# Kernel tuning notes

Measured on AMD Instinct MI355X. Metric: run time of the kernel, lower is better.

## Reference

```python
import jax, jax.numpy as jnp
import numpy as np

FEAT_DIM = 128
TIME_DIM = 128
D_MODEL = FEAT_DIM + TIME_DIM  # 256
N_HEAD = 2
D_K = D_MODEL // N_HEAD  # 128
B, N = 4096, 64


def setup_inputs() -> dict:
    key = jax.random.key(0)
    ks = jax.random.split(key, 16)
    s = lambda k, sh, sc=0.05: jax.random.normal(k, sh, dtype=jnp.float32) * sc
    return {
        "src": jax.random.normal(ks[0], (B, FEAT_DIM), dtype=jnp.float32),
        "src_t": jax.random.normal(ks[1], (B, 1, TIME_DIM), dtype=jnp.float32),
        "seq": jax.random.normal(ks[2], (B, N, FEAT_DIM), dtype=jnp.float32),
        "seq_t": jax.random.normal(ks[3], (B, N, TIME_DIM), dtype=jnp.float32),
        "mask": jax.random.randint(ks[4], (B, N), 0, 2).astype(jnp.bool_),
        # attention params (x @ W convention, W: [d_model, n_head*d_k])
        "w_qs": s(ks[5], (D_MODEL, N_HEAD * D_K)),
        "w_ks": s(ks[6], (D_MODEL, N_HEAD * D_K)),
        "w_vs": s(ks[7], (D_MODEL, N_HEAD * D_K)),
        "fc_w": s(ks[8], (N_HEAD * D_K, D_MODEL)),
        "fc_b": jnp.zeros((D_MODEL,), jnp.float32),
        "ln_g": jnp.ones((D_MODEL,), jnp.float32),
        "ln_b": jnp.zeros((D_MODEL,), jnp.float32),
        # MergeLayer params: fc1 [(d_model+feat), feat], fc2 [feat, feat]
        "fc1_w": s(ks[9], (D_MODEL + FEAT_DIM, FEAT_DIM)),
        "fc1_b": jnp.zeros((FEAT_DIM,), jnp.float32),
        "fc2_w": s(ks[10], (FEAT_DIM, FEAT_DIM)),
        "fc2_b": jnp.zeros((FEAT_DIM,), jnp.float32),
    }


def _layer_norm(x, g, b, eps=1e-5):
    mu = jnp.mean(x, axis=-1, keepdims=True)
    var = jnp.mean((x - mu) ** 2, axis=-1, keepdims=True)
    return (x - mu) * jax.lax.rsqrt(var + eps) * g + b


def reference(src, src_t, seq, seq_t, mask,
              w_qs, w_ks, w_vs, fc_w, fc_b, ln_g, ln_b,
              fc1_w, fc1_b, fc2_w, fc2_b):
    # q: [B,1,D_MODEL] = cat(src, src_t); k=v: [B,N,D_MODEL]
    q_in = jnp.concatenate([src[:, None, :], src_t], axis=2)
    k_in = jnp.concatenate([seq, seq_t], axis=2)

    q = (q_in @ w_qs).reshape(B, 1, N_HEAD, D_K)   # [B,1,H,dk]
    k = (k_in @ w_ks).reshape(B, N, N_HEAD, D_K)   # [B,N,H,dk]
    v = (k_in @ w_vs).reshape(B, N, N_HEAD, D_K)   # [B,N,H,dv]

    # scaled dot-product attention, len_q == 1
    attn = jnp.einsum('bqhd,bkhd->bhqk', q, k) / jnp.sqrt(jnp.float32(D_K))
    attn = jnp.where(mask[:, None, None, :], jnp.float32(-1e10), attn)
    attn = jax.nn.softmax(attn, axis=-1)           # [B,H,1,N]

    out = jnp.einsum('bhqk,bkhd->bqhd', attn, v).reshape(B, 1, N_HEAD * D_K)
    out = out @ fc_w + fc_b                         # dropout is identity (eval)
    out = _layer_norm(out + q_in, ln_g, ln_b)       # [B,1,D_MODEL]

    out = out[:, 0, :]                              # squeeze -> [B,D_MODEL]
    # MergeLayer: cat(out, src) -> fc1 -> relu -> fc2
    h = jnp.concatenate([out, src], axis=1)
    h = jax.nn.relu(h @ fc1_w + fc1_b)
    merged = h @ fc2_w + fc2_b                      # [B, FEAT_DIM]

    # attn squeeze: [n_head*B, N] ordering matches torch view(n_head, B, ...)
    attn_sq = jnp.transpose(attn[:, :, 0, :], (1, 0, 2)).reshape(N_HEAD * B, N)
    return merged, attn_sq
```

## Files before the change

### kernel.cpp

```cpp
#include <hip/hip_runtime.h>


__device__ __forceinline__ void fma4(float4& a, float s, const float4& w) {
  a.x = fmaf(s, w.x, a.x); a.y = fmaf(s, w.y, a.y);
  a.z = fmaf(s, w.z, a.z); a.w = fmaf(s, w.w, a.w);
}
__device__ __forceinline__ float dot4(const float4& a, const float4& b) {
  return a.x * b.x + a.y * b.y + a.z * b.z + a.w * b.w;
}

__global__ __launch_bounds__(256) void k_qproj(const float* __restrict__ src,
                                               const float* __restrict__ srct,
                                               const float* __restrict__ w_qs,
                                               float* __restrict__ Q) {
  __shared__ float sQ[16 * 256];
  const int tid = threadIdx.x;
  const int rb = blockIdx.x * 16;
  {
    const int r = tid >> 4;
    const int cb = (tid & 15) * 16;
#pragma unroll
    for (int i = 0; i < 4; ++i) {
      const int c = cb + i * 4;
      float4 v = (c < 128) ? *(const float4*)&src[(rb + r) * 128 + c]
                           : *(const float4*)&srct[(rb + r) * 128 + (c - 128)];
      *(float4*)&sQ[r * 256 + c] = v;
    }
  }
  __syncthreads();
  const int rg = tid >> 6;
  const int cg = tid & 63;
  float4 acc[4] = {};
  for (int k = 0; k < 256; k += 4) {
    const float4 w0 = *(const float4*)&w_qs[(k + 0) * 256 + cg * 4];
    const float4 w1 = *(const float4*)&w_qs[(k + 1) * 256 + cg * 4];
    const float4 w2 = *(const float4*)&w_qs[(k + 2) * 256 + cg * 4];
    const float4 w3 = *(const float4*)&w_qs[(k + 3) * 256 + cg * 4];
#pragma unroll
    for (int r = 0; r < 4; ++r) {
      const float4 a = *(const float4*)&sQ[(rg * 4 + r) * 256 + k];
      fma4(acc[r], a.x, w0); fma4(acc[r], a.y, w1);
      fma4(acc[r], a.z, w2); fma4(acc[r], a.w, w3);
    }
  }
#pragma unroll
  for (int r = 0; r < 4; ++r)
    *(float4*)&Q[(rb + rg * 4 + r) * 256 + cg * 4] = acc[r];
}

__global__ __launch_bounds__(256) void k_qkproj(const float* __restrict__ Q,
                                                const float* __restrict__ w_ks,
                                                float* __restrict__ QK) {
  __shared__ float sQ[8 * 256];
  const int tid = threadIdx.x;
  const int rb = blockIdx.x * 8;
#pragma unroll
  for (int i = 0; i < 2; ++i) {
    const int f4 = i * 256 + tid;
    const int r = f4 >> 6;
    const int c = (f4 & 63) * 4;
    *(float4*)&sQ[r * 256 + c] = *(const float4*)&Q[(rb + r) * 256 + c];
  }
  __syncthreads();
  const int rg = tid >> 7;
  const int cg = tid & 127;
  const int h = cg >> 6;
  const int j0 = (cg * 4) & 255;
  float4 acc[4] = {};
  for (int t = 0; t < 128; t += 4) {
    const float4 w0 = *(const float4*)&w_ks[(j0 + 0) * 256 + h * 128 + t];
    const float4 w1 = *(const float4*)&w_ks[(j0 + 1) * 256 + h * 128 + t];
    const float4 w2 = *(const float4*)&w_ks[(j0 + 2) * 256 + h * 128 + t];
    const float4 w3 = *(const float4*)&w_ks[(j0 + 3) * 256 + h * 128 + t];
#pragma unroll
    for (int r = 0; r < 4; ++r) {
      const float4 a = *(const float4*)&sQ[(rg * 4 + r) * 256 + h * 128 + t];
      acc[r].x += dot4(a, w0);
      acc[r].y += dot4(a, w1);
      acc[r].z += dot4(a, w2);
      acc[r].w += dot4(a, w3);
    }
  }
#pragma unroll
  for (int r = 0; r < 4; ++r)
    *(float4*)&QK[(rb + rg * 4 + r) * 512 + cg * 4] = acc[r];
}

__global__ __launch_bounds__(256) void k_attn(const float* __restrict__ seq,
                                              const float* __restrict__ seqt,
                                              const unsigned int* __restrict__ mw,
                                              float* QKS,
                                              float* __restrict__ att) {
  const int tid = threadIdx.x;
  const int lane = tid & 63;
  const int b = blockIdx.x * 4 + (tid >> 6);
  const int mv = (mw[b * 64 + lane] != 0u) ? 1 : 0;
  const float* kin = (lane < 32) ? (seq + b * 8192 + lane * 4)
                                 : (seqt + b * 8192 + (lane - 32) * 4);
  const float4 qk0 = *(const float4*)(QKS + b * 512 + lane * 4);
  const float4 qk1 = *(const float4*)(QKS + b * 512 + 256 + lane * 4);
  float4 s0 = {0.f, 0.f, 0.f, 0.f}, s1 = {0.f, 0.f, 0.f, 0.f};
  float l0 = 0.f, l1 = 0.f, rex0 = 0.f, rex1 = 0.f;
  const float scale = 0.08838834764831845f;
#pragma unroll 8
  for (int n = 0; n < 64; ++n) {
    const float4 kv = *(const float4*)(kin + n * 128);
    float p0 = dot4(kv, qk0);
    float p1 = dot4(kv, qk1);
#pragma unroll
    for (int off = 32; off >= 1; off >>= 1) {
      p0 += __shfl_xor(p0, off);
      p1 += __shfl_xor(p1, off);
    }
    const int mn = __shfl(mv, n);
    const float e0 = mn ? 0.f : __expf(p0 * scale);
    const float e1 = mn ? 0.f : __expf(p1 * scale);
    l0 += e0; l1 += e1;
    fma4(s0, e0, kv);
    fma4(s1, e1, kv);
    rex0 = (lane == n) ? e0 : rex0;
    rex1 = (lane == n) ? e1 : rex1;
  }
  const float i0 = 1.0f / l0;
  const float i1 = 1.0f / l1;
  const float4 o0 = {s0.x * i0, s0.y * i0, s0.z * i0, s0.w * i0};
  const float4 o1 = {s1.x * i1, s1.y * i1, s1.z * i1, s1.w * i1};
  *(float4*)(QKS + b * 512 + lane * 4) = o0;
  *(float4*)(QKS + b * 512 + 256 + lane * 4) = o1;
  att[b * 64 + lane] = rex0 * i0;
  att[4096 * 64 + b * 64 + lane] = rex1 * i1;
}

__global__ __launch_bounds__(256) void k_epi(
    const float* __restrict__ S, const float* __restrict__ src,
    const float* __restrict__ srct, const float* __restrict__ w_vs,
    const float* __restrict__ fc_w, const float* __restrict__ fc_b,
    const float* __restrict__ ln_g, const float* __restrict__ ln_b,
    const float* __restrict__ fc1_w, const float* __restrict__ fc1_b,
    const float* __restrict__ fc2_w, const float* __restrict__ fc2_b,
    float* __restrict__ out) {
  __shared__ float sv[4][512];
  __shared__ float qin[4][256];
  __shared__ float ov[4][256];
  __shared__ float xx[4][256];
  __shared__ float hcat[4][384];
  __shared__ float h1[4][128];
  __shared__ float stats[4][2];
  const int tid = threadIdx.x;
  const int b0 = blockIdx.x * 4;

#pragma unroll
  for (int i = 0; i < 2; ++i) {
    const int f4 = i * 256 + tid;
    const int g = f4 >> 7;
    const int c = (f4 & 127) * 4;
    *(float4*)&sv[g][c] = *(const float4*)&S[(b0 + g) * 512 + c];
  }
  {
    const int g = tid >> 6;
    const int c = (tid & 63) * 4;
    float4 v = (c < 128) ? *(const float4*)&src[(b0 + g) * 128 + c]
                         : *(const float4*)&srct[(b0 + g) * 128 + (c - 128)];
    *(float4*)&qin[g][c] = v;
  }
  __syncthreads();

  {
    const int h = tid >> 7;
    float acc[4] = {0.f, 0.f, 0.f, 0.f};
    for (int t = 0; t < 256; ++t) {
      const float w = w_vs[t * 256 + tid];
#pragma unroll
      for (int g = 0; g < 4; ++g) acc[g] = fmaf(sv[g][h * 256 + t], w, acc[g]);
    }
#pragma unroll
    for (int g = 0; g < 4; ++g) ov[g][tid] = acc[g];
  }
  __syncthreads();

  {
    float acc[4] = {0.f, 0.f, 0.f, 0.f};
    for (int d = 0; d < 256; ++d) {
      const float w = fc_w[d * 256 + tid];
#pragma unroll
      for (int g = 0; g < 4; ++g) acc[g] = fmaf(ov[g][d], w, acc[g]);
    }
    const float fb = fc_b[tid];
#pragma unroll
    for (int g = 0; g < 4; ++g) xx[g][tid] = acc[g] + fb + qin[g][tid];
  }
  __syncthreads();

  if (tid < 4) {
    const int g = tid;
    float s = 0.f, ss = 0.f;
    for (int j = 0; j < 256; ++j) {
      const float x = xx[g][j];
      s += x; ss += x * x;
    }
    const float mu = s * (1.0f / 256.0f);
    const float var = ss * (1.0f / 256.0f) - mu * mu;
    stats[g][0] = mu;
    stats[g][1] = rsqrtf(var + 1e-5f);
  }
  __syncthreads();
  {
    const float gg = ln_g[tid], bb = ln_b[tid];
#pragma unroll
    for (int g = 0; g < 4; ++g)
      hcat[g][tid] = (xx[g][tid] - stats[g][0]) * stats[g][1] * gg + bb;
  }
#pragma unroll
  for (int i = 0; i < 2; ++i) {
    const int idx = i * 256 + tid;
    const int g = idx >> 7, c = idx & 127;
    hcat[g][256 + c] = src[(b0 + g) * 128 + c];
  }
  __syncthreads();

  {
    const int col = tid & 127;
    const int gp = (tid >> 7) * 2;
    float acc0 = fc1_b[col], acc1 = acc0;
    for (int d = 0; d < 384; ++d) {
      const float w = fc1_w[d * 128 + col];
      acc0 = fmaf(hcat[gp][d], w, acc0);
      acc1 = fmaf(hcat[gp + 1][d], w, acc1);
    }
    h1[gp][col] = fmaxf(acc0, 0.f);
    h1[gp + 1][col] = fmaxf(acc1, 0.f);
  }
  __syncthreads();

  {
    const int col = tid & 127;
    const int gp = (tid >> 7) * 2;
    float acc0 = fc2_b[col], acc1 = acc0;
    for (int d = 0; d < 128; ++d) {
      const float w = fc2_w[d * 128 + col];
      acc0 = fmaf(h1[gp][d], w, acc0);
      acc1 = fmaf(h1[gp + 1][d], w, acc1);
    }
    out[(b0 + gp) * 128 + col] = acc0;
    out[(b0 + gp + 1) * 128 + col] = acc1;
  }
}

extern "C" void kernel_launch(void* const* d_in, const int* in_sizes, int n_in,
                              void* d_out, int out_size, void* d_ws,
                              size_t ws_size, hipStream_t stream) {
  (void)in_sizes; (void)n_in; (void)out_size; (void)ws_size;
  const float* src = (const float*)d_in[0];
  const float* srct = (const float*)d_in[1];
  const float* seq = (const float*)d_in[2];
  const float* seqt = (const float*)d_in[3];
  const unsigned int* mask = (const unsigned int*)d_in[4];
  const float* w_qs = (const float*)d_in[5];
  const float* w_ks = (const float*)d_in[6];
  const float* w_vs = (const float*)d_in[7];
  const float* fc_w = (const float*)d_in[8];
  const float* fc_b = (const float*)d_in[9];
  const float* ln_g = (const float*)d_in[10];
  const float* ln_b = (const float*)d_in[11];
  const float* fc1_w = (const float*)d_in[12];
  const float* fc1_b = (const float*)d_in[13];
  const float* fc2_w = (const float*)d_in[14];
  const float* fc2_b = (const float*)d_in[15];
  float* out = (float*)d_out;
  float* att = out + 4096 * 128;
  float* Q = (float*)d_ws;
  float* QKS = Q + 4096 * 256;
  k_qproj<<<256, 256, 0, stream>>>(src, srct, w_qs, Q);
  k_qkproj<<<512, 256, 0, stream>>>(Q, w_ks, QKS);
  k_attn<<<1024, 256, 0, stream>>>(seq, seqt, mask, QKS, att);
  k_epi<<<1024, 256, 0, stream>>>(QKS, src, srct, w_vs, fc_w, fc_b, ln_g,
                                  ln_b, fc1_w, fc1_b, fc2_w, fc2_b, out);
}
```

Baseline: 466.6 us.

## Fold Wq·Wkᵀ into one weight and restructure attention to skip masked keys

Precomputes a fused 256x512 weight W = Wq_h·Wk_hᵀ·scale per call, so the query-key projection becomes a single GEMM from the concatenated inputs instead of two chained projections. The attention kernel now computes each key's score with one lane per key (no per-key wave reductions), normalizes once, and accumulates the weighted sum only over unmasked keys using a ballot-compacted index list. This removes the 64 serial shuffle reductions per row and roughly halves the value-accumulation loads for the random mask, at the cost of an extra small weight-fusion kernel and strided per-lane row reads in the score pass. The softmax omits max-subtraction, which the old code also did.

```diff
diff --git a/kernel.cpp b/kernel.cpp
--- a/kernel.cpp
+++ b/kernel.cpp
@@ -9,13 +9,31 @@
   return a.x * b.x + a.y * b.y + a.z * b.z + a.w * b.w;
 }
 
-__global__ __launch_bounds__(256) void k_qproj(const float* __restrict__ src,
-                                               const float* __restrict__ srct,
-                                               const float* __restrict__ w_qs,
-                                               float* __restrict__ Q) {
+__global__ __launch_bounds__(256) void k_wf(const float* __restrict__ w_qs,
+                                            const float* __restrict__ w_ks,
+                                            float* __restrict__ W) {
+  const int idx = blockIdx.x * 256 + threadIdx.x;
+  const int c = idx >> 9;
+  const int col = idx & 511;
+  const int h = col >> 8;
+  const int j = col & 255;
+  const float* a = w_qs + c * 256 + h * 128;
+  const float* bk = w_ks + j * 256 + h * 128;
+  float acc = 0.f;
+#pragma unroll
+  for (int d = 0; d < 128; d += 4)
+    acc += dot4(*(const float4*)&a[d], *(const float4*)&bk[d]);
+  W[idx] = acc * 0.08838834764831845f;
+}
+
+__global__ __launch_bounds__(256) void k_qk(const float* __restrict__ src,
+                                            const float* __restrict__ srct,
+                                            const float* __restrict__ W,
+                                            float* __restrict__ QK) {
   __shared__ float sQ[16 * 256];
   const int tid = threadIdx.x;
-  const int rb = blockIdx.x * 16;
+  const int rb = (blockIdx.x >> 1) * 16;
+  const int ch = (blockIdx.x & 1) * 256;
   {
     const int r = tid >> 4;
     const int cb = (tid & 15) * 16;
@@ -30,12 +48,13 @@
   __syncthreads();
   const int rg = tid >> 6;
   const int cg = tid & 63;
+  const int col = ch + cg * 4;
   float4 acc[4] = {};
   for (int k = 0; k < 256; k += 4) {
-    const float4 w0 = *(const float4*)&w_qs[(k + 0) * 256 + cg * 4];
-    const float4 w1 = *(const float4*)&w_qs[(k + 1) * 256 + cg * 4];
-    const float4 w2 = *(const float4*)&w_qs[(k + 2) * 256 + cg * 4];
-    const float4 w3 = *(const float4*)&w_qs[(k + 3) * 256 + cg * 4];
+    const float4 w0 = *(const float4*)&W[(k + 0) * 512 + col];
+    const float4 w1 = *(const float4*)&W[(k + 1) * 512 + col];
+    const float4 w2 = *(const float4*)&W[(k + 2) * 512 + col];
+    const float4 w3 = *(const float4*)&W[(k + 3) * 512 + col];
 #pragma unroll
     for (int r = 0; r < 4; ++r) {
       const float4 a = *(const float4*)&sQ[(rg * 4 + r) * 256 + k];
@@ -45,45 +64,7 @@
   }
 #pragma unroll
   for (int r = 0; r < 4; ++r)
-    *(float4*)&Q[(rb + rg * 4 + r) * 256 + cg * 4] = acc[r];
-}
-
-__global__ __launch_bounds__(256) void k_qkproj(const float* __restrict__ Q,
-                                                const float* __restrict__ w_ks,
-                                                float* __restrict__ QK) {
-  __shared__ float sQ[8 * 256];
-  const int tid = threadIdx.x;
-  const int rb = blockIdx.x * 8;
-#pragma unroll
-  for (int i = 0; i < 2; ++i) {
-    const int f4 = i * 256 + tid;
-    const int r = f4 >> 6;
-    const int c = (f4 & 63) * 4;
-    *(float4*)&sQ[r * 256 + c] = *(const float4*)&Q[(rb + r) * 256 + c];
-  }
-  __syncthreads();
-  const int rg = tid >> 7;
-  const int cg = tid & 127;
-  const int h = cg >> 6;
-  const int j0 = (cg * 4) & 255;
-  float4 acc[4] = {};
-  for (int t = 0; t < 128; t += 4) {
-    const float4 w0 = *(const float4*)&w_ks[(j0 + 0) * 256 + h * 128 + t];
-    const float4 w1 = *(const float4*)&w_ks[(j0 + 1) * 256 + h * 128 + t];
-    const float4 w2 = *(const float4*)&w_ks[(j0 + 2) * 256 + h * 128 + t];
-    const float4 w3 = *(const float4*)&w_ks[(j0 + 3) * 256 + h * 128 + t];
-#pragma unroll
-    for (int r = 0; r < 4; ++r) {
-      const float4 a = *(const float4*)&sQ[(rg * 4 + r) * 256 + h * 128 + t];
-      acc[r].x += dot4(a, w0);
-      acc[r].y += dot4(a, w1);
-      acc[r].z += dot4(a, w2);
-      acc[r].w += dot4(a, w3);
-    }
-  }
-#pragma unroll
-  for (int r = 0; r < 4; ++r)
-    *(float4*)&QK[(rb + rg * 4 + r) * 512 + cg * 4] = acc[r];
+    *(float4*)&QK[(rb + rg * 4 + r) * 512 + col] = acc[r];
 }
 
 __global__ __launch_bounds__(256) void k_attn(const float* __restrict__ seq,
@@ -91,44 +72,88 @@
                                               const unsigned int* __restrict__ mw,
                                               float* QKS,
                                               float* __restrict__ att) {
+  __shared__ float sqk[4][512];
+  __shared__ float se0[4][64];
+  __shared__ float se1[4][64];
+  __shared__ int nlist[4][64];
   const int tid = threadIdx.x;
   const int lane = tid & 63;
-  const int b = blockIdx.x * 4 + (tid >> 6);
-  const int mv = (mw[b * 64 + lane] != 0u) ? 1 : 0;
+  const int w = tid >> 6;
+  const int b0 = blockIdx.x * 4;
+  const int b = b0 + w;
+#pragma unroll
+  for (int i = 0; i < 2; ++i) {
+    const int f4 = i * 256 + tid;
+    const int g = f4 >> 7;
+    const int c = (f4 & 127) * 4;
+    *(float4*)&sqk[g][c] = *(const float4*)&QKS[(b0 + g) * 512 + c];
+  }
+  __syncthreads();
+
+  const bool masked = (mw[b * 64 + lane] != 0u);
+  const float* srow = seq + b * 8192 + lane * 128;
+  const float* trow = seqt + b * 8192 + lane * 128;
+  float p0s = 0.f, p0t = 0.f, p1s = 0.f, p1t = 0.f;
+  if (!masked) {
+#pragma unroll 4
+    for (int i = 0; i < 32; ++i) {
+      const float4 ks = *(const float4*)&srow[i * 4];
+      const float4 kt = *(const float4*)&trow[i * 4];
+      const float4 q0s = *(const float4*)&sqk[w][i * 4];
+      const float4 q0t = *(const float4*)&sqk[w][128 + i * 4];
+      const float4 q1s = *(const float4*)&sqk[w][256 + i * 4];
+      const float4 q1t = *(const float4*)&sqk[w][384 + i * 4];
+      p0s += dot4(ks, q0s); p0t += dot4(kt, q0t);
+      p1s += dot4(ks, q1s); p1t += dot4(kt, q1t);
+    }
+  }
+  const float e0 = masked ? 0.f : __expf(p0s + p0t);
+  const float e1 = masked ? 0.f : __expf(p1s + p1t);
+  float l0 = e0, l1 = e1;
+#pragma unroll
+  for (int off = 32; off >= 1; off >>= 1) {
+    l0 += __shfl_xor(l0, off);
+    l1 += __shfl_xor(l1, off);
+  }
+  const float a0 = e0 / l0;
+  const float a1 = e1 / l1;
+  att[b * 64 + lane] = a0;
+  att[4096 * 64 + b * 64 + lane] = a1;
+
+  const unsigned long long bits = __ballot(!masked);
+  const int cnt = __popcll(bits);
+  const int pos = __popcll(bits & ((1ull << lane) - 1ull));
+  if (!masked) nlist[w][pos] = lane;
+  se0[w][lane] = a0;
+  se1[w][lane] = a1;
+  __syncthreads();
+
   const float* kin = (lane < 32) ? (seq + b * 8192 + lane * 4)
                                  : (seqt + b * 8192 + (lane - 32) * 4);
-  const float4 qk0 = *(const float4*)(QKS + b * 512 + lane * 4);
-  const float4 qk1 = *(const float4*)(QKS + b * 512 + 256 + lane * 4);
   float4 s0 = {0.f, 0.f, 0.f, 0.f}, s1 = {0.f, 0.f, 0.f, 0.f};
-  float l0 = 0.f, l1 = 0.f, rex0 = 0.f, rex1 = 0.f;
-  const float scale = 0.08838834764831845f;
-#pragma unroll 8
-  for (int n = 0; n < 64; ++n) {
+  int t = 0;
+  for (; t + 4 <= cnt; t += 4) {
+    const int n0 = nlist[w][t + 0];
+    const int n1 = nlist[w][t + 1];
+    const int n2 = nlist[w][t + 2];
+    const int n3 = nlist[w][t + 3];
+    const float4 k0 = *(const float4*)(kin + n0 * 128);
+    const float4 k1 = *(const float4*)(kin + n1 * 128);
+    const float4 k2 = *(const float4*)(kin + n2 * 128);
+    const float4 k3 = *(const float4*)(kin + n3 * 128);
+    fma4(s0, se0[w][n0], k0); fma4(s1, se1[w][n0], k0);
+    fma4(s0, se0[w][n1], k1); fma4(s1, se1[w][n1], k1);
+    fma4(s0, se0[w][n2], k2); fma4(s1, se1[w][n2], k2);
+    fma4(s0, se0[w][n3], k3); fma4(s1, se1[w][n3], k3);
+  }
+  for (; t < cnt; ++t) {
+    const int n = nlist[w][t];
     const float4 kv = *(const float4*)(kin + n * 128);
-    float p0 = dot4(kv, qk0);
-    float p1 = dot4(kv, qk1);
-#pragma unroll
-    for (int off = 32; off >= 1; off >>= 1) {
-      p0 += __shfl_xor(p0, off);
-      p1 += __shfl_xor(p1, off);
-    }
-    const int mn = __shfl(mv, n);
-    const float e0 = mn ? 0.f : __expf(p0 * scale);
-    const float e1 = mn ? 0.f : __expf(p1 * scale);
-    l0 += e0; l1 += e1;
-    fma4(s0, e0, kv);
-    fma4(s1, e1, kv);
-    rex0 = (lane == n) ? e0 : rex0;
-    rex1 = (lane == n) ? e1 : rex1;
-  }
-  const float i0 = 1.0f / l0;
-  const float i1 = 1.0f / l1;
-  const float4 o0 = {s0.x * i0, s0.y * i0, s0.z * i0, s0.w * i0};
-  const float4 o1 = {s1.x * i1, s1.y * i1, s1.z * i1, s1.w * i1};
-  *(float4*)(QKS + b * 512 + lane * 4) = o0;
-  *(float4*)(QKS + b * 512 + 256 + lane * 4) = o1;
-  att[b * 64 + lane] = rex0 * i0;
-  att[4096 * 64 + b * 64 + lane] = rex1 * i1;
+    fma4(s0, se0[w][n], kv);
+    fma4(s1, se1[w][n], kv);
+  }
+  *(float4*)(QKS + b * 512 + lane * 4) = s0;
+  *(float4*)(QKS + b * 512 + 256 + lane * 4) = s1;
 }
 
 __global__ __launch_bounds__(256) void k_epi(
@@ -268,10 +293,10 @@
   const float* fc2_b = (const float*)d_in[15];
   float* out = (float*)d_out;
   float* att = out + 4096 * 128;
-  float* Q = (float*)d_ws;
-  float* QKS = Q + 4096 * 256;
-  k_qproj<<<256, 256, 0, stream>>>(src, srct, w_qs, Q);
-  k_qkproj<<<512, 256, 0, stream>>>(Q, w_ks, QKS);
+  float* W = (float*)d_ws;
+  float* QKS = W + 256 * 512;
+  k_wf<<<512, 256, 0, stream>>>(w_qs, w_ks, W);
+  k_qk<<<512, 256, 0, stream>>>(src, srct, W, QKS);
   k_attn<<<1024, 256, 0, stream>>>(seq, seqt, mask, QKS, att);
   k_epi<<<1024, 256, 0, stream>>>(QKS, src, srct, w_vs, fc_w, fc_b, ln_g,
                                   ln_b, fc1_w, fc1_b, fc2_w, fc2_b, out);
```

New measurement: 432.9 us. 1.08x faster.
